# Optimization experiments

Measured on AMD Instinct MI355X. Metric: run time of the kernel, lower is better.

## Reference

```python
import jax, jax.numpy as jnp
import numpy as np

N_NODES = 50000


def _gcn_norm(edge_index, num_nodes):
    # add self loops, compute symmetric normalization D^-1/2 (A+I) D^-1/2
    loops = jnp.arange(num_nodes, dtype=edge_index.dtype)
    row = jnp.concatenate([edge_index[0], loops])
    col = jnp.concatenate([edge_index[1], loops])
    deg = jax.ops.segment_sum(jnp.ones_like(row, dtype=jnp.float32), col,
                              num_segments=num_nodes)
    dinv = jnp.where(deg > 0, jax.lax.rsqrt(deg), 0.0)
    norm = dinv[row] * dinv[col]  # [E']
    return row, col, norm


def _gcn_conv(x, W, b, row, col, norm, num_nodes):
    h = x @ W                       # [N, out] transform first (smaller dim)
    msg = h[row] * norm[:, None]    # gather along source nodes  [E', out]
    agg = jax.ops.segment_sum(msg, col, num_segments=num_nodes)  # scatter-add
    return agg + b


def setup_inputs() -> dict:
    key = jax.random.key(0)
    k1, k2, k3, k4 = jax.random.split(key, 4)
    x = jax.random.normal(k1, (N_NODES, 128), dtype=jnp.float32)
    edge_index = jax.random.randint(k2, (2, 800000), 0, N_NODES, dtype=jnp.int64)
    W1 = jax.random.normal(k3, (128, 128), dtype=jnp.float32) * (1.0 / np.sqrt(128))
    b1 = jnp.zeros((128,), dtype=jnp.float32)
    W2 = jax.random.normal(k4, (128, 16), dtype=jnp.float32) * (1.0 / np.sqrt(128))
    b2 = jnp.zeros((16,), dtype=jnp.float32)
    return {"x": x, "edge_index": edge_index, "W1": W1, "b1": b1, "W2": W2, "b2": b2}


def reference(x, edge_index, W1, b1, W2, b2):
    n = x.shape[0]
    row, col, norm = _gcn_norm(edge_index, n)
    h = _gcn_conv(x, W1, b1, row, col, norm, n)
    h = jax.nn.relu(h)
    h = _gcn_conv(h, W2, b2, row, col, norm, n)
    return jax.nn.log_softmax(h, axis=1)
```

## Files before the change

kernel.cpp:

```cpp
#include <hip/hip_runtime.h>
#include <math.h>

constexpr int N  = 50000;
constexpr int E  = 800000;
constexpr int F1 = 128;
constexpr int F2 = 16;
constexpr int BSHIFT  = 8;
constexpr int NBUCKET = (N + 255) >> BSHIFT;
constexpr int CHUNK   = 2048;
constexpr int CAP     = 6144;
constexpr int SBLK    = (E + CHUNK - 1) / CHUNK;
constexpr int GBLK    = 391;

typedef unsigned short ushort_t;
typedef unsigned char  uchar_t;
typedef __bf16 bf16x8 __attribute__((ext_vector_type(8)));
typedef float  f32x4  __attribute__((ext_vector_type(4)));

static __device__ __forceinline__ float blo(unsigned u) { return __uint_as_float(u << 16); }
static __device__ __forceinline__ float bhi(unsigned u) { return __uint_as_float(u & 0xffff0000u); }
static __device__ __forceinline__ ushort_t to_bf(float f) { __bf16 h = (__bf16)f; return *(ushort_t*)&h; }
static __device__ __forceinline__ uchar_t to_fp8(float f) {
    return (uchar_t)(__builtin_amdgcn_cvt_pk_fp8_f32(f, f, 0, false) & 0xff);
}
static __device__ __forceinline__ float fp8lo(unsigned u) { return __builtin_amdgcn_cvt_f32_fp8(u, 0); }
static __device__ __forceinline__ float fp8hi(unsigned u) { return __builtin_amdgcn_cvt_f32_fp8(u, 1); }

__global__ __launch_bounds__(256) void k_scatterP_gemm1(const int* __restrict__ row,
                                                        const int* __restrict__ col,
                                                        int* __restrict__ cursor,
                                                        unsigned* __restrict__ P,
                                                        const float* __restrict__ x,
                                                        const float* __restrict__ W1,
                                                        uchar_t* __restrict__ h1q) {
    __shared__ ushort_t Wl[F1 * 136];
    int t = threadIdx.x;

    if (blockIdx.x < SBLK) {
        int* hist = (int*)Wl;
        int* cur  = hist + NBUCKET;
        if (t < NBUCKET) hist[t] = 0;
        __syncthreads();
        int base = blockIdx.x * CHUNK;
#pragma unroll
        for (int i = 0; i < CHUNK / 256; ++i) {
            int e = base + i * 256 + t;
            if (e < E) atomicAdd(&hist[col[e] >> BSHIFT], 1);
        }
        __syncthreads();
        if (t < NBUCKET) cur[t] = t * CAP + atomicAdd(&cursor[t], hist[t]);
        __syncthreads();
#pragma unroll
        for (int i = 0; i < CHUNK / 256; ++i) {
            int e = base + i * 256 + t;
            if (e < E) {
                int c = col[e];
                int pos = atomicAdd(&cur[c >> BSHIFT], 1);
                P[pos] = ((unsigned)row[e] << BSHIFT) | (unsigned)(c & 255);
            }
        }
        return;
    }

    int gb = blockIdx.x - SBLK;
    {
        int n = t & 127, kh = t >> 7;
#pragma unroll
        for (int j = 0; j < 8; ++j) {
            int k0 = (kh * 8 + j) * 8;
            bf16x8 w;
#pragma unroll
            for (int i2 = 0; i2 < 8; ++i2) w[i2] = (__bf16)W1[(k0 + i2) * F1 + n];
            *(bf16x8*)&Wl[n * 136 + k0] = w;
        }
    }
    __syncthreads();

    int lane = t & 63, wv = t >> 6;
    int quad = lane >> 4, l15 = lane & 15;
#pragma unroll 1
    for (int tile = gb * 2; tile < gb * 2 + 2; ++tile) {
        int arow = tile * 64 + wv * 16 + l15;
        int rclamp = min(arow, N - 1);
        f32x4 acc[8] = {};
#pragma unroll
        for (int kk = 0; kk < 4; ++kk) {
            int k0 = kk * 32 + quad * 8;
            const float* xp = x + (size_t)rclamp * F1 + k0;
            float4 u0 = *(const float4*)xp;
            float4 u1 = *(const float4*)(xp + 4);
            bf16x8 a;
            a[0] = (__bf16)u0.x; a[1] = (__bf16)u0.y; a[2] = (__bf16)u0.z; a[3] = (__bf16)u0.w;
            a[4] = (__bf16)u1.x; a[5] = (__bf16)u1.y; a[6] = (__bf16)u1.z; a[7] = (__bf16)u1.w;
#pragma unroll
            for (int ct = 0; ct < 8; ++ct) {
                bf16x8 b = *(const bf16x8*)&Wl[(ct * 16 + l15) * 136 + k0];
                acc[ct] = __builtin_amdgcn_mfma_f32_16x16x32_bf16(a, b, acc[ct], 0, 0, 0);
            }
        }
        int orow0 = tile * 64 + wv * 16 + quad * 4;
#pragma unroll
        for (int r = 0; r < 4; ++r) {
            int orow = orow0 + r;
            if (orow < N) {
#pragma unroll
                for (int ct = 0; ct < 8; ++ct)
                    h1q[(size_t)orow * F1 + ct * 16 + l15] = to_fp8(acc[ct][r]);
            }
        }
    }
}

__global__ __launch_bounds__(512) void k_binFinal(const unsigned* __restrict__ P,
                                                  const int* __restrict__ cursor,
                                                  ushort_t* __restrict__ csr16,
                                                  int* __restrict__ seg_start,
                                                  int* __restrict__ counts,
                                                  float* __restrict__ dinv) {
    __shared__ unsigned eb[CAP];
    __shared__ int cnt[256];
    __shared__ int cur[256];
    __shared__ int wtot[4];
    int t = threadIdx.x;
    int b = blockIdx.x;
    int lo = b << BSHIFT;
    int n_nodes = min(256, N - lo);
    int m = cursor[b];
    if (t < 256) cnt[t] = 0;
    __syncthreads();
    const unsigned* Pb = P + (size_t)b * CAP;
    for (int k = t; k < m; k += 512) {
        unsigned u = Pb[k];
        eb[k] = u;
        atomicAdd(&cnt[u & 255], 1);
    }
    __syncthreads();
    int lane = t & 63, wid = t >> 6;
    int v = 0, incl = 0;
    if (t < 256) {
        v = cnt[t];
        incl = v;
#pragma unroll
        for (int d = 1; d < 64; d <<= 1) {
            int u = __shfl_up(incl, d, 64);
            if (lane >= d) incl += u;
        }
        if (lane == 63) wtot[wid] = incl;
    }
    __syncthreads();
    if (t < 256) {
        int wb = 0;
        for (int w = 0; w < wid; ++w) wb += wtot[w];
        int o = b * CAP + wb + incl - v;
        cur[t] = o;
        if (t < n_nodes) {
            seg_start[lo + t] = o;
            counts[lo + t] = v;
            dinv[lo + t] = rsqrtf((float)v + 1.f);
        }
    }
    __syncthreads();
    for (int k = t; k < m; k += 512) {
        unsigned u = eb[k];
        int pos = atomicAdd(&cur[u & 255], 1);
        csr16[pos] = (ushort_t)(u >> BSHIFT);
    }
}

__global__ __launch_bounds__(256) void k_gather1_gemm2(const uchar_t* __restrict__ h1q,
                                                       const int* __restrict__ seg_start,
                                                       const int* __restrict__ counts,
                                                       const ushort_t* __restrict__ csr16,
                                                       const float* __restrict__ dinv,
                                                       const float* __restrict__ W2,
                                                       const float* __restrict__ b1,
                                                       ushort_t* __restrict__ h2s) {
    __shared__ ushort_t W2l[F2 * 136];
    __shared__ ushort_t T[16 * 136];
    __shared__ float dv[16];
    int t = threadIdx.x;
    for (int i = t; i < F1 * F2; i += 256) {
        int k = i >> 4, n = i & 15;
        W2l[n * 136 + k] = to_bf(W2[i]);
    }
    int lane = t & 63, wv = t >> 6;
    float2 bb = ((const float2*)b1)[lane];
    int nbase = blockIdx.x * 16;

#pragma unroll 1
    for (int i = 0; i < 4; ++i) {
        int nl = wv * 4 + i;
        int c = nbase + nl;
        unsigned pw = 0u;
        float dc = 0.f;
        if (c < N) {
            dc = dinv[c];
            int s = seg_start[c], e = s + counts[c];
            float ax = 0.f, ay = 0.f;
            int k = s;
            for (; k + 4 <= e; k += 4) {
                int r0 = csr16[k], r1 = csr16[k + 1], r2 = csr16[k + 2], r3 = csr16[k + 3];
                float d0 = dinv[r0], d1 = dinv[r1], d2 = dinv[r2], d3 = dinv[r3];
                unsigned u0 = ((const ushort_t*)(h1q + (size_t)r0 * F1))[lane];
                unsigned u1 = ((const ushort_t*)(h1q + (size_t)r1 * F1))[lane];
                unsigned u2 = ((const ushort_t*)(h1q + (size_t)r2 * F1))[lane];
                unsigned u3 = ((const ushort_t*)(h1q + (size_t)r3 * F1))[lane];
                ax = fmaf(d0, fp8lo(u0), ax); ay = fmaf(d0, fp8hi(u0), ay);
                ax = fmaf(d1, fp8lo(u1), ax); ay = fmaf(d1, fp8hi(u1), ay);
                ax = fmaf(d2, fp8lo(u2), ax); ay = fmaf(d2, fp8hi(u2), ay);
                ax = fmaf(d3, fp8lo(u3), ax); ay = fmaf(d3, fp8hi(u3), ay);
            }
            for (; k < e; ++k) {
                int r0 = csr16[k];
                float d0 = dinv[r0];
                unsigned u0 = ((const ushort_t*)(h1q + (size_t)r0 * F1))[lane];
                ax = fmaf(d0, fp8lo(u0), ax); ay = fmaf(d0, fp8hi(u0), ay);
            }
            unsigned us = ((const ushort_t*)(h1q + (size_t)c * F1))[lane];
            ax = fmaf(dc, fp8lo(us), ax); ay = fmaf(dc, fp8hi(us), ay);
            float o0 = fmaxf(fmaf(dc, ax, bb.x), 0.f);
            float o1 = fmaxf(fmaf(dc, ay, bb.y), 0.f);
            pw = (unsigned)to_bf(o0) | ((unsigned)to_bf(o1) << 16);
        }
        *(unsigned*)&T[nl * 136 + lane * 2] = pw;
        if (lane == 0) dv[nl] = dc;
    }
    __syncthreads();

    if (wv == 0) {
        int quad = lane >> 4, l15 = lane & 15;
        f32x4 acc = {};
#pragma unroll
        for (int kk = 0; kk < 4; ++kk) {
            int k0 = kk * 32 + quad * 8;
            bf16x8 a = *(const bf16x8*)&T[l15 * 136 + k0];
            bf16x8 b = *(const bf16x8*)&W2l[l15 * 136 + k0];
            acc = __builtin_amdgcn_mfma_f32_16x16x32_bf16(a, b, acc, 0, 0, 0);
        }
#pragma unroll
        for (int r = 0; r < 4; ++r) {
            int rw = quad * 4 + r;
            int gn = nbase + rw;
            if (gn < N) h2s[(size_t)gn * F2 + l15] = to_bf(acc[r] * dv[rw]);
        }
    }
}

__global__ __launch_bounds__(256) void k_gather2(const ushort_t* __restrict__ h2s,
                                                 const int* __restrict__ seg_start,
                                                 const int* __restrict__ counts,
                                                 const ushort_t* __restrict__ csr16,
                                                 const float* __restrict__ dinv,
                                                 const float* __restrict__ b2,
                                                 float* __restrict__ out) {
    int idx = blockIdx.x * 256 + threadIdx.x;
    int node = idx >> 3, sub = idx & 7;
    if (node >= N) return;
    int s = seg_start[node], e = s + counts[node];
    float ax = 0.f, ay = 0.f;
    int k = s;
    for (; k + 4 <= e; k += 4) {
        int r0 = csr16[k], r1 = csr16[k + 1], r2 = csr16[k + 2], r3 = csr16[k + 3];
        unsigned u0 = ((const unsigned*)(h2s + (size_t)r0 * F2))[sub];
        unsigned u1 = ((const unsigned*)(h2s + (size_t)r1 * F2))[sub];
        unsigned u2 = ((const unsigned*)(h2s + (size_t)r2 * F2))[sub];
        unsigned u3 = ((const unsigned*)(h2s + (size_t)r3 * F2))[sub];
        ax += (blo(u0) + blo(u1)) + (blo(u2) + blo(u3));
        ay += (bhi(u0) + bhi(u1)) + (bhi(u2) + bhi(u3));
    }
    for (; k < e; ++k) {
        unsigned u = ((const unsigned*)(h2s + (size_t)csr16[k] * F2))[sub];
        ax += blo(u);
        ay += bhi(u);
    }
    unsigned us = ((const unsigned*)(h2s + (size_t)node * F2))[sub];
    ax += blo(us);
    ay += bhi(us);
    float dc = dinv[node];
    float2 bb = ((const float2*)b2)[sub];
    float v0 = fmaf(dc, ax, bb.x);
    float v1 = fmaf(dc, ay, bb.y);
    float mx = fmaxf(v0, v1);
#pragma unroll
    for (int m = 1; m < 8; m <<= 1) mx = fmaxf(mx, __shfl_xor(mx, m));
    float sm = expf(v0 - mx) + expf(v1 - mx);
#pragma unroll
    for (int m = 1; m < 8; m <<= 1) sm += __shfl_xor(sm, m);
    float lse = mx + logf(sm);
    float2 o;
    o.x = v0 - lse;
    o.y = v1 - lse;
    ((float2*)(out + (size_t)node * F2))[sub] = o;
}

extern "C" void kernel_launch(void* const* d_in, const int* in_sizes, int n_in,
                              void* d_out, int out_size, void* d_ws, size_t ws_size,
                              hipStream_t stream) {
    const float* x  = (const float*)d_in[0];
    const int*   ei = (const int*)d_in[1];
    const float* W1 = (const float*)d_in[2];
    const float* b1 = (const float*)d_in[3];
    const float* W2 = (const float*)d_in[4];
    const float* b2 = (const float*)d_in[5];
    const int* row = ei;
    const int* col = ei + E;

    char* ws = (char*)d_ws;
    int*      cursor    = (int*)ws;      ws += 256 * 4;
    unsigned* P         = (unsigned*)ws; ws += (size_t)NBUCKET * CAP * 4;
    ushort_t* csr16     = (ushort_t*)ws; ws += (size_t)NBUCKET * CAP * 2;
    int*      seg_start = (int*)ws;      ws += (size_t)N * 4;
    int*      counts    = (int*)ws;      ws += (size_t)N * 4;
    float*    dinv      = (float*)ws;    ws += (size_t)N * 4;
    uchar_t*  h1q       = (uchar_t*)ws;  ws += (size_t)N * F1;
    ushort_t* h2s       = (ushort_t*)ws; ws += (size_t)N * F2 * 2;

    hipMemsetAsync(cursor, 0, 256 * 4, stream);

    k_scatterP_gemm1<<<SBLK + GBLK, 256, 0, stream>>>(row, col, cursor, P, x, W1, h1q);
    k_binFinal<<<NBUCKET, 512, 0, stream>>>(P, cursor, csr16, seg_start, counts, dinv);
    k_gather1_gemm2<<<(N + 15) / 16, 256, 0, stream>>>(h1q, seg_start, counts, csr16,
                                                       dinv, W2, b1, h2s);
    k_gather2<<<((size_t)N * 8 + 255) / 256, 256, 0, stream>>>(h2s, seg_start, counts, csr16,
                                                               dinv, b2, (float*)d_out);
}
```

Baseline: 160.1 us.

## Cooperatively load CSR indices and broadcast via shuffles in both gather kernels

In the first gather, a wave now loads up to 64 neighbor indices and their dinv values at once, one per lane, then broadcasts them with shuffles. Each half-wave handles alternate edges with 4-byte fp8 loads per lane, and the two halves are combined with a cross-half shuffle reduction. The second gather likewise has each 8-lane group load 8 indices together and shuffle them out, so the per-thread serial index and dinv loads are gone. This trades redundant scalar-dependent loads for shuffle instructions and extra masked work on tail edges.

```diff
diff --git a/kernel.cpp b/kernel.cpp
--- a/kernel.cpp
+++ b/kernel.cpp
@@ -23,8 +23,6 @@
 static __device__ __forceinline__ uchar_t to_fp8(float f) {
     return (uchar_t)(__builtin_amdgcn_cvt_pk_fp8_f32(f, f, 0, false) & 0xff);
 }
-static __device__ __forceinline__ float fp8lo(unsigned u) { return __builtin_amdgcn_cvt_f32_fp8(u, 0); }
-static __device__ __forceinline__ float fp8hi(unsigned u) { return __builtin_amdgcn_cvt_f32_fp8(u, 1); }
 
 __global__ __launch_bounds__(256) void k_scatterP_gemm1(const int* __restrict__ row,
                                                         const int* __restrict__ col,
@@ -184,47 +182,64 @@
         W2l[n * 136 + k] = to_bf(W2[i]);
     }
     int lane = t & 63, wv = t >> 6;
-    float2 bb = ((const float2*)b1)[lane];
+    int half = lane >> 5, q = lane & 31;
+    float4 bb = ((const float4*)b1)[q];
     int nbase = blockIdx.x * 16;
+
+#define G1LOAD(n_, u_) { int jj = j + half + 2 * (u_); int src = min(jj, rem - 1);          \
+        int r = __shfl(rl, src); float ee = __shfl(dl, src); if (jj >= rem) ee = 0.f;       \
+        w##n_ = *(const unsigned*)(h1q + (size_t)r * F1 + (q << 2)); e##n_ = ee; }
+#define G1ACC(n_) { a0 = fmaf(e##n_, __builtin_amdgcn_cvt_f32_fp8(w##n_, 0), a0);           \
+                    a1 = fmaf(e##n_, __builtin_amdgcn_cvt_f32_fp8(w##n_, 1), a1);           \
+                    a2 = fmaf(e##n_, __builtin_amdgcn_cvt_f32_fp8(w##n_, 2), a2);           \
+                    a3 = fmaf(e##n_, __builtin_amdgcn_cvt_f32_fp8(w##n_, 3), a3); }
 
 #pragma unroll 1
     for (int i = 0; i < 4; ++i) {
         int nl = wv * 4 + i;
         int c = nbase + nl;
-        unsigned pw = 0u;
+        float a0 = 0.f, a1 = 0.f, a2 = 0.f, a3 = 0.f;
         float dc = 0.f;
         if (c < N) {
             dc = dinv[c];
-            int s = seg_start[c], e = s + counts[c];
-            float ax = 0.f, ay = 0.f;
-            int k = s;
-            for (; k + 4 <= e; k += 4) {
-                int r0 = csr16[k], r1 = csr16[k + 1], r2 = csr16[k + 2], r3 = csr16[k + 3];
-                float d0 = dinv[r0], d1 = dinv[r1], d2 = dinv[r2], d3 = dinv[r3];
-                unsigned u0 = ((const ushort_t*)(h1q + (size_t)r0 * F1))[lane];
-                unsigned u1 = ((const ushort_t*)(h1q + (size_t)r1 * F1))[lane];
-                unsigned u2 = ((const ushort_t*)(h1q + (size_t)r2 * F1))[lane];
-                unsigned u3 = ((const ushort_t*)(h1q + (size_t)r3 * F1))[lane];
-                ax = fmaf(d0, fp8lo(u0), ax); ay = fmaf(d0, fp8hi(u0), ay);
-                ax = fmaf(d1, fp8lo(u1), ax); ay = fmaf(d1, fp8hi(u1), ay);
-                ax = fmaf(d2, fp8lo(u2), ax); ay = fmaf(d2, fp8hi(u2), ay);
-                ax = fmaf(d3, fp8lo(u3), ax); ay = fmaf(d3, fp8hi(u3), ay);
+            int s = seg_start[c];
+            int cntc = counts[c];
+            for (int s0 = 0; s0 < cntc; s0 += 64) {
+                int rem = min(cntc - s0, 64);
+                int rl = 0; float dl = 0.f;
+                if (lane < rem) { rl = csr16[s + s0 + lane]; dl = dinv[rl]; }
+#pragma unroll 1
+                for (int j = 0; j < rem; j += 16) {
+                    unsigned w0, w1, w2, w3, w4, w5, w6, w7;
+                    float e0, e1, e2, e3, e4, e5, e6, e7;
+                    G1LOAD(0, 0) G1LOAD(1, 1) G1LOAD(2, 2) G1LOAD(3, 3)
+                    G1LOAD(4, 4) G1LOAD(5, 5) G1LOAD(6, 6) G1LOAD(7, 7)
+                    G1ACC(0) G1ACC(1) G1ACC(2) G1ACC(3)
+                    G1ACC(4) G1ACC(5) G1ACC(6) G1ACC(7)
+                }
             }
-            for (; k < e; ++k) {
-                int r0 = csr16[k];
-                float d0 = dinv[r0];
-                unsigned u0 = ((const ushort_t*)(h1q + (size_t)r0 * F1))[lane];
-                ax = fmaf(d0, fp8lo(u0), ax); ay = fmaf(d0, fp8hi(u0), ay);
-            }
-            unsigned us = ((const ushort_t*)(h1q + (size_t)c * F1))[lane];
-            ax = fmaf(dc, fp8lo(us), ax); ay = fmaf(dc, fp8hi(us), ay);
-            float o0 = fmaxf(fmaf(dc, ax, bb.x), 0.f);
-            float o1 = fmaxf(fmaf(dc, ay, bb.y), 0.f);
-            pw = (unsigned)to_bf(o0) | ((unsigned)to_bf(o1) << 16);
-        }
-        *(unsigned*)&T[nl * 136 + lane * 2] = pw;
+            a0 += __shfl_xor(a0, 32); a1 += __shfl_xor(a1, 32);
+            a2 += __shfl_xor(a2, 32); a3 += __shfl_xor(a3, 32);
+            unsigned us = *(const unsigned*)(h1q + (size_t)c * F1 + (q << 2));
+            a0 = fmaf(dc, __builtin_amdgcn_cvt_f32_fp8(us, 0), a0);
+            a1 = fmaf(dc, __builtin_amdgcn_cvt_f32_fp8(us, 1), a1);
+            a2 = fmaf(dc, __builtin_amdgcn_cvt_f32_fp8(us, 2), a2);
+            a3 = fmaf(dc, __builtin_amdgcn_cvt_f32_fp8(us, 3), a3);
+            a0 = fmaxf(fmaf(dc, a0, bb.x), 0.f);
+            a1 = fmaxf(fmaf(dc, a1, bb.y), 0.f);
+            a2 = fmaxf(fmaf(dc, a2, bb.z), 0.f);
+            a3 = fmaxf(fmaf(dc, a3, bb.w), 0.f);
+        }
+        if (half == 0) {
+            unsigned p0 = (unsigned)to_bf(a0) | ((unsigned)to_bf(a1) << 16);
+            unsigned p1 = (unsigned)to_bf(a2) | ((unsigned)to_bf(a3) << 16);
+            uint2 pp; pp.x = p0; pp.y = p1;
+            *(uint2*)&T[nl * 136 + (q << 2)] = pp;
+        }
         if (lane == 0) dv[nl] = dc;
     }
+#undef G1LOAD
+#undef G1ACC
     __syncthreads();
 
     if (wv == 0) {
@@ -256,23 +271,28 @@
     int idx = blockIdx.x * 256 + threadIdx.x;
     int node = idx >> 3, sub = idx & 7;
     if (node >= N) return;
-    int s = seg_start[node], e = s + counts[node];
+    int lane = threadIdx.x & 63;
+    int gb = lane & 56;
+    int s = seg_start[node], cntc = counts[node];
     float ax = 0.f, ay = 0.f;
-    int k = s;
-    for (; k + 4 <= e; k += 4) {
-        int r0 = csr16[k], r1 = csr16[k + 1], r2 = csr16[k + 2], r3 = csr16[k + 3];
-        unsigned u0 = ((const unsigned*)(h2s + (size_t)r0 * F2))[sub];
-        unsigned u1 = ((const unsigned*)(h2s + (size_t)r1 * F2))[sub];
-        unsigned u2 = ((const unsigned*)(h2s + (size_t)r2 * F2))[sub];
-        unsigned u3 = ((const unsigned*)(h2s + (size_t)r3 * F2))[sub];
-        ax += (blo(u0) + blo(u1)) + (blo(u2) + blo(u3));
-        ay += (bhi(u0) + bhi(u1)) + (bhi(u2) + bhi(u3));
-    }
-    for (; k < e; ++k) {
-        unsigned u = ((const unsigned*)(h2s + (size_t)csr16[k] * F2))[sub];
-        ax += blo(u);
-        ay += bhi(u);
-    }
+
+#define G2LOAD(n_) { int src = gb | min(n_, rem - 1); int r = __shfl(rl, src);              \
+        w##n_ = ((const unsigned*)(h2s + (size_t)r * F2))[sub]; if (n_ >= rem) w##n_ = 0u; }
+
+#pragma unroll 1
+    for (int j0 = 0; j0 < cntc; j0 += 8) {
+        int rem = min(cntc - j0, 8);
+        int rl = 0;
+        if (sub < rem) rl = csr16[s + j0 + sub];
+        unsigned w0, w1, w2, w3, w4, w5, w6, w7;
+        G2LOAD(0) G2LOAD(1) G2LOAD(2) G2LOAD(3)
+        G2LOAD(4) G2LOAD(5) G2LOAD(6) G2LOAD(7)
+        ax += ((blo(w0) + blo(w1)) + (blo(w2) + blo(w3))) +
+              ((blo(w4) + blo(w5)) + (blo(w6) + blo(w7)));
+        ay += ((bhi(w0) + bhi(w1)) + (bhi(w2) + bhi(w3))) +
+              ((bhi(w4) + bhi(w5)) + (bhi(w6) + bhi(w7)));
+    }
+#undef G2LOAD
     unsigned us = ((const unsigned*)(h2s + (size_t)node * F2))[sub];
     ax += blo(us);
     ay += bhi(us);
```

Result: faster. 154.9 us (-3.2%).
